# Kernel optimization log

Hardware: AMD Instinct MI355X
Metric: run time of the kernel (lower is better)

The kernel has to match this reference:

```python
import jax, jax.numpy as jnp
import numpy as np

N_NODES = 200000
N_EDGES = 6400000
IN_FEAT = 128
HIDDEN = 16


def gcn_conv(x, W, b, row, col, n):
    # PyG GCNConv: h = X W ; out_i = sum_{(j->i)} d_j^{-1/2} d_i^{-1/2} h_j + b
    # (row = source j, col = target i; self-loops already included in row/col)
    deg = jax.ops.segment_sum(jnp.ones_like(col, dtype=x.dtype), col, num_segments=n)
    dinv = jnp.where(deg > 0, jax.lax.rsqrt(deg), jnp.zeros_like(deg))
    norm = dinv[row] * dinv[col]            # [E+N]
    h = x @ W                               # [N, out] small GEMM
    msg = norm[:, None] * h[row]            # gather over edges
    out = jax.ops.segment_sum(msg, col, num_segments=n)  # scatter-add to targets
    return out + b


def setup_inputs() -> dict:
    key = jax.random.key(0)
    k1, k2, k3, k4 = jax.random.split(key, 4)
    x = jax.random.normal(k1, (N_NODES, IN_FEAT), dtype=jnp.float32)
    edge_index = jax.random.randint(k2, (2, N_EDGES), 0, N_NODES, dtype=jnp.int32)
    # Glorot-ish init for the two linear layers
    W1 = jax.random.normal(k3, (IN_FEAT, HIDDEN), dtype=jnp.float32) / np.sqrt(IN_FEAT)
    W2 = jax.random.normal(k4, (HIDDEN, 1), dtype=jnp.float32) / np.sqrt(HIDDEN)
    b1 = jnp.zeros((HIDDEN,), dtype=jnp.float32)
    b2 = jnp.zeros((1,), dtype=jnp.float32)
    return {"x": x, "edge_index": edge_index, "W1": W1, "b1": b1, "W2": W2, "b2": b2}


def reference(x, edge_index, W1, b1, W2, b2):
    n = x.shape[0]
    # add self-loops (as PyG GCNConv does by default)
    loop = jnp.arange(n, dtype=edge_index.dtype)
    row = jnp.concatenate([edge_index[0], loop])
    col = jnp.concatenate([edge_index[1], loop])
    h = gcn_conv(x, W1, b1, row, col, n)    # [N, 16]
    h = jax.nn.relu(h)
    out = gcn_conv(h, W2, b2, row, col, n)  # [N, 1]
    return out.squeeze(-1)                  # [N]
```

## Files before the change

kernel.cpp:

```cpp
#include <hip/hip_runtime.h>
#include <hip/hip_fp16.h>

#define N_NODES 200000
#define N_EDGES 6400000
#define IN_FEAT 128
#define HIDDEN  16

#define RN 128
#define NRF 1568
#define NC 98
#define CSHIFT 11
#define NPAD (NRF * RN)
#define SRC_MASK 0x3FFFFu
#define SB1 8192
#define SB2 8192
#define BPB 9
#define CAP 5120

typedef float v4f __attribute__((ext_vector_type(4)));
typedef _Float16 f16x8 __attribute__((ext_vector_type(8)));
typedef float f32x4 __attribute__((ext_vector_type(4)));


__global__ __launch_bounds__(512) void k_fcnt(const int* __restrict__ col,
                                              unsigned* __restrict__ fcnt) {
    __shared__ unsigned c[NRF];
    for (int i = threadIdx.x; i < NRF; i += 512) c[i] = 0u;
    __syncthreads();
    const int EPB = N_EDGES / 512;
    const int4* c4 = (const int4*)(col + (size_t)blockIdx.x * EPB);
    for (int i = threadIdx.x; i < EPB / 4; i += 512) {
        int4 v = c4[i];
        atomicAdd(&c[(unsigned)v.x >> 7], 1u);
        atomicAdd(&c[(unsigned)v.y >> 7], 1u);
        atomicAdd(&c[(unsigned)v.z >> 7], 1u);
        atomicAdd(&c[(unsigned)v.w >> 7], 1u);
    }
    __syncthreads();
    for (int i = threadIdx.x; i < NRF; i += 512)
        if (c[i]) atomicAdd(&fcnt[i], c[i]);
}


__global__ __launch_bounds__(1024) void k_scanr(const unsigned* __restrict__ fcnt,
                                                unsigned* __restrict__ foffs,
                                                unsigned* __restrict__ fcur,
                                                unsigned* __restrict__ coffs,
                                                unsigned* __restrict__ ccur) {
    __shared__ unsigned s[1024];
    const int t = threadIdx.x;
    unsigned c0 = (2 * t     < NRF) ? fcnt[2 * t]     : 0u;
    unsigned c1 = (2 * t + 1 < NRF) ? fcnt[2 * t + 1] : 0u;
    unsigned pairsum = c0 + c1;
    s[t] = pairsum;
    __syncthreads();
    #pragma unroll
    for (int d = 1; d < 1024; d <<= 1) {
        unsigned add = (t >= d) ? s[t - d] : 0u;
        __syncthreads();
        s[t] += add;
        __syncthreads();
    }
    unsigned excl = s[t] - pairsum;
    if (2 * t < NRF)     { foffs[2 * t]     = excl;      fcur[2 * t]     = excl; }
    if (2 * t + 1 < NRF) { foffs[2 * t + 1] = excl + c0; fcur[2 * t + 1] = excl + c0; }
    if (t == 1023) foffs[NRF] = s[t];
    __syncthreads();
    if (t < NC)  { unsigned v = foffs[16 * t]; coffs[t] = v; ccur[t] = v; }
    if (t == NC) coffs[NC] = N_EDGES;
}


__global__ __launch_bounds__(512) void k_cscat(const int* __restrict__ row,
                                               const int* __restrict__ col,
                                               unsigned* __restrict__ ccur,
                                               unsigned* __restrict__ tmp1) {
    __shared__ unsigned cnt[NC], gbase[NC], lcur[NC];
    const long long e0 = (long long)blockIdx.x * SB1;
    long long rem = (long long)N_EDGES - e0;
    const int n = rem > SB1 ? SB1 : (int)rem;
    if (threadIdx.x < NC) { cnt[threadIdx.x] = 0u; lcur[threadIdx.x] = 0u; }
    __syncthreads();
    const int4* c4 = (const int4*)(col + e0);
    const int4* r4 = (const int4*)(row + e0);
    for (int i = threadIdx.x; i < n / 4; i += 512) {
        int4 v = c4[i];
        atomicAdd(&cnt[(unsigned)v.x >> CSHIFT], 1u);
        atomicAdd(&cnt[(unsigned)v.y >> CSHIFT], 1u);
        atomicAdd(&cnt[(unsigned)v.z >> CSHIFT], 1u);
        atomicAdd(&cnt[(unsigned)v.w >> CSHIFT], 1u);
    }
    __syncthreads();
    if (threadIdx.x < NC)
        gbase[threadIdx.x] = cnt[threadIdx.x] ? atomicAdd(&ccur[threadIdx.x], cnt[threadIdx.x]) : 0u;
    __syncthreads();
    for (int i = threadIdx.x; i < n / 4; i += 512) {
        int4 c = c4[i];
        int4 r = r4[i];
        unsigned b, pos;
        b = (unsigned)c.x >> CSHIFT; pos = gbase[b] + atomicAdd(&lcur[b], 1u);
        tmp1[pos] = (((unsigned)c.x & 2047u) << 18) | (unsigned)r.x;
        b = (unsigned)c.y >> CSHIFT; pos = gbase[b] + atomicAdd(&lcur[b], 1u);
        tmp1[pos] = (((unsigned)c.y & 2047u) << 18) | (unsigned)r.y;
        b = (unsigned)c.z >> CSHIFT; pos = gbase[b] + atomicAdd(&lcur[b], 1u);
        tmp1[pos] = (((unsigned)c.z & 2047u) << 18) | (unsigned)r.z;
        b = (unsigned)c.w >> CSHIFT; pos = gbase[b] + atomicAdd(&lcur[b], 1u);
        tmp1[pos] = (((unsigned)c.w & 2047u) << 18) | (unsigned)r.w;
    }
}


__global__ __launch_bounds__(512) void k_fscat(const unsigned* __restrict__ tmp1,
                                               const unsigned* __restrict__ coffs,
                                               unsigned* __restrict__ fcur,
                                               unsigned* __restrict__ tmp2) {
    __shared__ unsigned cnt[16], gbase[16], lcur[16];
    const int b = blockIdx.x / BPB;
    const int sl = blockIdx.x % BPB;
    const unsigned blo = coffs[b], bhi = coffs[b + 1];
    const unsigned lo = blo + (unsigned)sl * SB2;
    if (lo >= bhi) return;
    const unsigned hi = (lo + SB2 < bhi) ? lo + SB2 : bhi;
    const unsigned n = hi - lo;
    if (threadIdx.x < 16) { cnt[threadIdx.x] = 0u; lcur[threadIdx.x] = 0u; }
    __syncthreads();
    for (unsigned i = threadIdx.x; i < n; i += 512)
        atomicAdd(&cnt[tmp1[lo + i] >> 25], 1u);
    __syncthreads();
    if (threadIdx.x < 16)
        gbase[threadIdx.x] = cnt[threadIdx.x]
            ? atomicAdd(&fcur[16 * b + threadIdx.x], cnt[threadIdx.x]) : 0u;
    __syncthreads();
    for (unsigned i = threadIdx.x; i < n; i += 512) {
        unsigned p = tmp1[lo + i];
        unsigned f = p >> 25;
        unsigned pos = gbase[f] + atomicAdd(&lcur[f], 1u);
        tmp2[pos] = p & 0x01FFFFFFu;
    }
}


__global__ __launch_bounds__(256) void k_bsort(const unsigned* __restrict__ tmp,
                                               const unsigned* __restrict__ boffs_r,
                                               unsigned* __restrict__ boffs_n,
                                               float* __restrict__ dinv,
                                               unsigned* __restrict__ sorted) {
    __shared__ unsigned obuf[CAP];
    __shared__ unsigned dcnt[RN], dcur[RN], sscan[RN];
    const int r = blockIdx.x;
    const unsigned lo = boffs_r[r], hi = boffs_r[r + 1];
    const unsigned cnt = hi - lo;
    const unsigned node0 = (unsigned)r * RN;
    if (threadIdx.x < RN) dcnt[threadIdx.x] = 0u;
    __syncthreads();

    for (unsigned i = threadIdx.x; i < cnt; i += 256)
        atomicAdd(&dcnt[tmp[lo + i] >> 18], 1u);
    __syncthreads();

    unsigned c = 0;
    if (threadIdx.x < RN) { c = dcnt[threadIdx.x]; sscan[threadIdx.x] = c; }
    __syncthreads();
    #pragma unroll
    for (int d = 1; d < RN; d <<= 1) {
        unsigned add = 0;
        if (threadIdx.x < RN && threadIdx.x >= d) add = sscan[threadIdx.x - d];
        __syncthreads();
        if (threadIdx.x < RN) sscan[threadIdx.x] += add;
        __syncthreads();
    }
    if (threadIdx.x < RN) {
        unsigned excl = sscan[threadIdx.x] - c;
        dcur[threadIdx.x] = excl;
        unsigned node = node0 + threadIdx.x;
        boffs_n[node] = lo + excl;
        if (node < N_NODES) dinv[node] = rsqrtf((float)c + 1.0f);
    }
    if (r == NRF - 1 && threadIdx.x == 0) boffs_n[NPAD] = hi;
    __syncthreads();

    if (cnt <= CAP) {
        for (unsigned i = threadIdx.x; i < cnt; i += 256) {
            unsigned p = tmp[lo + i];
            unsigned pos = atomicAdd(&dcur[p >> 18], 1u);
            obuf[pos] = p & SRC_MASK;
        }
        __syncthreads();
        for (unsigned i = threadIdx.x; i < cnt; i += 256)
            sorted[lo + i] = obuf[i];
    } else {
        for (unsigned i = threadIdx.x; i < cnt; i += 256) {
            unsigned p = tmp[lo + i];
            unsigned pos = atomicAdd(&dcur[p >> 18], 1u);
            sorted[lo + pos] = p & SRC_MASK;
        }
    }
}


__global__ __launch_bounds__(256) void k_gemm1(const float* __restrict__ x,
                                               const float* __restrict__ W1,
                                               const float* __restrict__ dinv,
                                               __half* __restrict__ h16) {
    const int wave = (blockIdx.x * 256 + threadIdx.x) >> 6;
    const int lane = threadIdx.x & 63;
    const int m16 = lane & 15;
    const int quad = lane >> 4;
    if (wave * 16 >= N_NODES) return;

    f16x8 bf[4];
    #pragma unroll
    for (int kb = 0; kb < 4; ++kb)
        #pragma unroll
        for (int j = 0; j < 8; ++j)
            bf[kb][j] = (_Float16)W1[(kb * 32 + quad * 8 + j) * HIDDEN + m16];

    const int node0 = wave * 16;
    const float* xrow = x + (size_t)(node0 + m16) * IN_FEAT + quad * 8;
    f32x4 acc = {0.f, 0.f, 0.f, 0.f};
    #pragma unroll
    for (int kb = 0; kb < 4; ++kb) {
        const v4f* p = (const v4f*)(xrow + kb * 32);
        v4f u0 = p[0], u1 = p[1];
        f16x8 af;
        af[0] = (_Float16)u0.x; af[1] = (_Float16)u0.y;
        af[2] = (_Float16)u0.z; af[3] = (_Float16)u0.w;
        af[4] = (_Float16)u1.x; af[5] = (_Float16)u1.y;
        af[6] = (_Float16)u1.z; af[7] = (_Float16)u1.w;
        acc = __builtin_amdgcn_mfma_f32_16x16x32_f16(af, bf[kb], acc, 0, 0, 0);
    }
    #pragma unroll
    for (int r = 0; r < 4; ++r) {
        int node = node0 + quad * 4 + r;
        h16[(size_t)node * HIDDEN + m16] = __float2half(dinv[node] * acc[r]);
    }
}


__global__ __launch_bounds__(256) void k_agg1(const unsigned* __restrict__ sorted,
                                              const unsigned* __restrict__ boffs,
                                              const unsigned* __restrict__ h16u,
                                              const float* __restrict__ dinv,
                                              const float* __restrict__ b1,
                                              const float* __restrict__ W2,
                                              float* __restrict__ tp) {
    const unsigned tid = blockIdx.x * 256 + threadIdx.x;
    const unsigned node = tid >> 3;
    const int l = tid & 7;
    if (node >= N_NODES) return;

    unsigned e = boffs[node];
    const unsigned o1 = boffs[node + 1];
    float ax = 0.f, ay = 0.f;

    unsigned n0, n1, n2, n3, n4, n5, n6, n7;
    bool have = (e + 8 <= o1);
    if (have) {
        n0 = sorted[e];     n1 = sorted[e + 1]; n2 = sorted[e + 2]; n3 = sorted[e + 3];
        n4 = sorted[e + 4]; n5 = sorted[e + 5]; n6 = sorted[e + 6]; n7 = sorted[e + 7];
    }
    while (have) {
        unsigned c0 = n0, c1 = n1, c2 = n2, c3 = n3, c4 = n4, c5 = n5, c6 = n6, c7 = n7;
        e += 8;
        have = (e + 8 <= o1);
        if (have) {
            n0 = sorted[e];     n1 = sorted[e + 1]; n2 = sorted[e + 2]; n3 = sorted[e + 3];
            n4 = sorted[e + 4]; n5 = sorted[e + 5]; n6 = sorted[e + 6]; n7 = sorted[e + 7];
        }
        unsigned v0 = h16u[(size_t)c0 * 8 + l];
        unsigned v1 = h16u[(size_t)c1 * 8 + l];
        unsigned v2 = h16u[(size_t)c2 * 8 + l];
        unsigned v3 = h16u[(size_t)c3 * 8 + l];
        unsigned v4 = h16u[(size_t)c4 * 8 + l];
        unsigned v5 = h16u[(size_t)c5 * 8 + l];
        unsigned v6 = h16u[(size_t)c6 * 8 + l];
        unsigned v7 = h16u[(size_t)c7 * 8 + l];
        float2 f0 = __half22float2(*(const __half2*)&v0);
        float2 f1 = __half22float2(*(const __half2*)&v1);
        float2 f2 = __half22float2(*(const __half2*)&v2);
        float2 f3 = __half22float2(*(const __half2*)&v3);
        float2 f4 = __half22float2(*(const __half2*)&v4);
        float2 f5 = __half22float2(*(const __half2*)&v5);
        float2 f6 = __half22float2(*(const __half2*)&v6);
        float2 f7 = __half22float2(*(const __half2*)&v7);
        ax += f0.x + f1.x + f2.x + f3.x;
        ay += f0.y + f1.y + f2.y + f3.y;
        ax += f4.x + f5.x + f6.x + f7.x;
        ay += f4.y + f5.y + f6.y + f7.y;
    }
    for (; e < o1; ++e) {
        unsigned s = sorted[e];
        unsigned v = h16u[(size_t)s * 8 + l];
        float2 f = __half22float2(*(const __half2*)&v);
        ax += f.x; ay += f.y;
    }

    unsigned vs = h16u[(size_t)node * 8 + l];
    float2 fs = __half22float2(*(const __half2*)&vs);
    float di = dinv[node];
    float px = fmaf(di, ax + fs.x, b1[2 * l]);
    float py = fmaf(di, ay + fs.y, b1[2 * l + 1]);
    float r = fmaxf(px, 0.f) * W2[2 * l] + fmaxf(py, 0.f) * W2[2 * l + 1];
    r += __shfl_xor(r, 4, 8);
    r += __shfl_xor(r, 2, 8);
    r += __shfl_xor(r, 1, 8);
    if (l == 0) tp[node] = di * r;
}


__global__ __launch_bounds__(256) void k_agg2(const unsigned* __restrict__ sorted,
                                              const unsigned* __restrict__ boffs,
                                              const float* __restrict__ tp,
                                              const float* __restrict__ dinv,
                                              const float* __restrict__ b2,
                                              float* __restrict__ out) {
    const unsigned node = blockIdx.x * 256 + threadIdx.x;
    if (node >= N_NODES) return;

    unsigned e = boffs[node];
    const unsigned o1 = boffs[node + 1];
    float acc = 0.f;

    unsigned n0, n1, n2, n3, n4, n5, n6, n7;
    bool have = (e + 8 <= o1);
    if (have) {
        n0 = sorted[e];     n1 = sorted[e + 1]; n2 = sorted[e + 2]; n3 = sorted[e + 3];
        n4 = sorted[e + 4]; n5 = sorted[e + 5]; n6 = sorted[e + 6]; n7 = sorted[e + 7];
    }
    while (have) {
        unsigned c0 = n0, c1 = n1, c2 = n2, c3 = n3, c4 = n4, c5 = n5, c6 = n6, c7 = n7;
        e += 8;
        have = (e + 8 <= o1);
        if (have) {
            n0 = sorted[e];     n1 = sorted[e + 1]; n2 = sorted[e + 2]; n3 = sorted[e + 3];
            n4 = sorted[e + 4]; n5 = sorted[e + 5]; n6 = sorted[e + 6]; n7 = sorted[e + 7];
        }
        float t0 = tp[c0], t1 = tp[c1], t2 = tp[c2], t3 = tp[c3];
        float t4 = tp[c4], t5 = tp[c5], t6 = tp[c6], t7 = tp[c7];
        acc += t0 + t1 + t2 + t3;
        acc += t4 + t5 + t6 + t7;
    }
    for (; e < o1; ++e) acc += tp[sorted[e]];

    out[node] = fmaf(dinv[node], tp[node] + acc, b2[0]);
}


extern "C" void kernel_launch(void* const* d_in, const int* in_sizes, int n_in,
                              void* d_out, int out_size, void* d_ws, size_t ws_size,
                              hipStream_t stream) {
    const float* x   = (const float*)d_in[0];
    const int*   ei  = (const int*)d_in[1];
    const float* W1  = (const float*)d_in[2];
    const float* b1  = (const float*)d_in[3];
    const float* W2  = (const float*)d_in[4];
    const float* b2  = (const float*)d_in[5];
    float* out = (float*)d_out;

    const int* row = ei;
    const int* col = ei + N_EDGES;

    unsigned* fcnt    = (unsigned*)d_ws;
    unsigned* foffs   = fcnt + 2048;
    unsigned* fcur    = foffs + 2048;
    unsigned* coffs   = fcur + 2048;
    unsigned* ccur    = coffs + 128;
    unsigned* boffs_n = ccur + 128;
    float*    dinv    = (float*)(boffs_n + NPAD + 64);
    float*    tp      = dinv + N_NODES;
    __half*   h16     = (__half*)(tp + N_NODES);
    unsigned* tmp1    = (unsigned*)(h16 + (size_t)N_NODES * HIDDEN);
    unsigned* tmp2    = tmp1 + N_EDGES;
    unsigned* sorted  = tmp1;

    (void)hipMemsetAsync(fcnt, 0, 2048 * sizeof(unsigned), stream);
    k_fcnt<<<512, 512, 0, stream>>>(col, fcnt);
    k_scanr<<<1, 1024, 0, stream>>>(fcnt, foffs, fcur, coffs, ccur);
    k_cscat<<<(N_EDGES + SB1 - 1) / SB1, 512, 0, stream>>>(row, col, ccur, tmp1);
    k_fscat<<<NC * BPB, 512, 0, stream>>>(tmp1, coffs, fcur, tmp2);
    k_bsort<<<NRF, 256, 0, stream>>>(tmp2, foffs, boffs_n, dinv, sorted);
    k_gemm1<<<(N_NODES / 16 + 3) / 4, 256, 0, stream>>>(x, W1, dinv, h16);
    k_agg1<<<(N_NODES * 8) / 256 + 1, 256, 0, stream>>>(sorted, boffs_n, (const unsigned*)h16,
                                                        dinv, b1, W2, tp);
    k_agg2<<<(N_NODES + 255) / 256, 256, 0, stream>>>(sorted, boffs_n, tp, dinv, b2, out);
}
```

Before: 409.8 us.

## Collapse three-level radix sort into two passes with 512-node buckets

Replaces the coarse-scatter / fine-scatter / per-128-node sort pipeline with a two-pass scheme: edges are scattered into 391 buckets of 512 target nodes, then one 1024-thread block per bucket counts per node and scatters sources directly to global memory. This removes one full read and write pass over the edge array and a kernel launch. The scatter kernel also keeps the loaded col/row vectors in registers between counting and writing instead of re-reading them. The cost is fewer, larger sort blocks (391) with uncoalesced global writes instead of LDS staging, plus more buckets contending on atomics in the coarse scatter.

```diff
diff --git a/kernel.cpp b/kernel.cpp
--- a/kernel.cpp
+++ b/kernel.cpp
@@ -6,68 +6,54 @@
 #define IN_FEAT 128
 #define HIDDEN  16
 
-#define RN 128
-#define NRF 1568
-#define NC 98
-#define CSHIFT 11
-#define NPAD (NRF * RN)
+#define RN 512
+#define CSHIFT 9
+#define NC 391
+#define NPAD (NC * RN)
 #define SRC_MASK 0x3FFFFu
-#define SB1 8192
-#define SB2 8192
-#define BPB 9
-#define CAP 5120
+#define SB1 4096
 
 typedef float v4f __attribute__((ext_vector_type(4)));
 typedef _Float16 f16x8 __attribute__((ext_vector_type(8)));
 typedef float f32x4 __attribute__((ext_vector_type(4)));
 
 
-__global__ __launch_bounds__(512) void k_fcnt(const int* __restrict__ col,
-                                              unsigned* __restrict__ fcnt) {
-    __shared__ unsigned c[NRF];
-    for (int i = threadIdx.x; i < NRF; i += 512) c[i] = 0u;
+__global__ __launch_bounds__(512) void k_ccnt(const int* __restrict__ col,
+                                              unsigned* __restrict__ ccnt) {
+    __shared__ unsigned c[NC];
+    if (threadIdx.x < NC) c[threadIdx.x] = 0u;
     __syncthreads();
     const int EPB = N_EDGES / 512;
     const int4* c4 = (const int4*)(col + (size_t)blockIdx.x * EPB);
     for (int i = threadIdx.x; i < EPB / 4; i += 512) {
         int4 v = c4[i];
-        atomicAdd(&c[(unsigned)v.x >> 7], 1u);
-        atomicAdd(&c[(unsigned)v.y >> 7], 1u);
-        atomicAdd(&c[(unsigned)v.z >> 7], 1u);
-        atomicAdd(&c[(unsigned)v.w >> 7], 1u);
-    }
-    __syncthreads();
-    for (int i = threadIdx.x; i < NRF; i += 512)
-        if (c[i]) atomicAdd(&fcnt[i], c[i]);
-}
-
-
-__global__ __launch_bounds__(1024) void k_scanr(const unsigned* __restrict__ fcnt,
-                                                unsigned* __restrict__ foffs,
-                                                unsigned* __restrict__ fcur,
-                                                unsigned* __restrict__ coffs,
-                                                unsigned* __restrict__ ccur) {
-    __shared__ unsigned s[1024];
+        atomicAdd(&c[(unsigned)v.x >> CSHIFT], 1u);
+        atomicAdd(&c[(unsigned)v.y >> CSHIFT], 1u);
+        atomicAdd(&c[(unsigned)v.z >> CSHIFT], 1u);
+        atomicAdd(&c[(unsigned)v.w >> CSHIFT], 1u);
+    }
+    __syncthreads();
+    if (threadIdx.x < NC && c[threadIdx.x]) atomicAdd(&ccnt[threadIdx.x], c[threadIdx.x]);
+}
+
+
+__global__ __launch_bounds__(512) void k_scanc(const unsigned* __restrict__ ccnt,
+                                               unsigned* __restrict__ coffs,
+                                               unsigned* __restrict__ ccur) {
+    __shared__ unsigned s[512];
     const int t = threadIdx.x;
-    unsigned c0 = (2 * t     < NRF) ? fcnt[2 * t]     : 0u;
-    unsigned c1 = (2 * t + 1 < NRF) ? fcnt[2 * t + 1] : 0u;
-    unsigned pairsum = c0 + c1;
-    s[t] = pairsum;
-    __syncthreads();
-    #pragma unroll
-    for (int d = 1; d < 1024; d <<= 1) {
+    unsigned v = (t < NC) ? ccnt[t] : 0u;
+    s[t] = v;
+    __syncthreads();
+    #pragma unroll
+    for (int d = 1; d < 512; d <<= 1) {
         unsigned add = (t >= d) ? s[t - d] : 0u;
         __syncthreads();
         s[t] += add;
         __syncthreads();
     }
-    unsigned excl = s[t] - pairsum;
-    if (2 * t < NRF)     { foffs[2 * t]     = excl;      fcur[2 * t]     = excl; }
-    if (2 * t + 1 < NRF) { foffs[2 * t + 1] = excl + c0; fcur[2 * t + 1] = excl + c0; }
-    if (t == 1023) foffs[NRF] = s[t];
-    __syncthreads();
-    if (t < NC)  { unsigned v = foffs[16 * t]; coffs[t] = v; ccur[t] = v; }
-    if (t == NC) coffs[NC] = N_EDGES;
+    if (t < NC) { unsigned e = s[t] - v; coffs[t] = e; ccur[t] = e; }
+    if (t == NC - 1) coffs[NC] = s[t];
 }
 
 
@@ -83,8 +69,13 @@
     __syncthreads();
     const int4* c4 = (const int4*)(col + e0);
     const int4* r4 = (const int4*)(row + e0);
-    for (int i = threadIdx.x; i < n / 4; i += 512) {
+    const int n4 = n / 4;
+    int4 cc[2], rr[2];
+    int nit = 0;
+    for (int i = threadIdx.x; i < n4; i += 512, ++nit) {
         int4 v = c4[i];
+        cc[nit] = v;
+        rr[nit] = r4[i];
         atomicAdd(&cnt[(unsigned)v.x >> CSHIFT], 1u);
         atomicAdd(&cnt[(unsigned)v.y >> CSHIFT], 1u);
         atomicAdd(&cnt[(unsigned)v.z >> CSHIFT], 1u);
@@ -94,68 +85,36 @@
     if (threadIdx.x < NC)
         gbase[threadIdx.x] = cnt[threadIdx.x] ? atomicAdd(&ccur[threadIdx.x], cnt[threadIdx.x]) : 0u;
     __syncthreads();
-    for (int i = threadIdx.x; i < n / 4; i += 512) {
-        int4 c = c4[i];
-        int4 r = r4[i];
+    for (int it = 0; it < nit; ++it) {
+        int4 c = cc[it];
+        int4 r = rr[it];
         unsigned b, pos;
         b = (unsigned)c.x >> CSHIFT; pos = gbase[b] + atomicAdd(&lcur[b], 1u);
-        tmp1[pos] = (((unsigned)c.x & 2047u) << 18) | (unsigned)r.x;
+        tmp1[pos] = (((unsigned)c.x & (RN - 1u)) << 18) | (unsigned)r.x;
         b = (unsigned)c.y >> CSHIFT; pos = gbase[b] + atomicAdd(&lcur[b], 1u);
-        tmp1[pos] = (((unsigned)c.y & 2047u) << 18) | (unsigned)r.y;
+        tmp1[pos] = (((unsigned)c.y & (RN - 1u)) << 18) | (unsigned)r.y;
         b = (unsigned)c.z >> CSHIFT; pos = gbase[b] + atomicAdd(&lcur[b], 1u);
-        tmp1[pos] = (((unsigned)c.z & 2047u) << 18) | (unsigned)r.z;
+        tmp1[pos] = (((unsigned)c.z & (RN - 1u)) << 18) | (unsigned)r.z;
         b = (unsigned)c.w >> CSHIFT; pos = gbase[b] + atomicAdd(&lcur[b], 1u);
-        tmp1[pos] = (((unsigned)c.w & 2047u) << 18) | (unsigned)r.w;
-    }
-}
-
-
-__global__ __launch_bounds__(512) void k_fscat(const unsigned* __restrict__ tmp1,
-                                               const unsigned* __restrict__ coffs,
-                                               unsigned* __restrict__ fcur,
-                                               unsigned* __restrict__ tmp2) {
-    __shared__ unsigned cnt[16], gbase[16], lcur[16];
-    const int b = blockIdx.x / BPB;
-    const int sl = blockIdx.x % BPB;
-    const unsigned blo = coffs[b], bhi = coffs[b + 1];
-    const unsigned lo = blo + (unsigned)sl * SB2;
-    if (lo >= bhi) return;
-    const unsigned hi = (lo + SB2 < bhi) ? lo + SB2 : bhi;
-    const unsigned n = hi - lo;
-    if (threadIdx.x < 16) { cnt[threadIdx.x] = 0u; lcur[threadIdx.x] = 0u; }
-    __syncthreads();
-    for (unsigned i = threadIdx.x; i < n; i += 512)
-        atomicAdd(&cnt[tmp1[lo + i] >> 25], 1u);
-    __syncthreads();
-    if (threadIdx.x < 16)
-        gbase[threadIdx.x] = cnt[threadIdx.x]
-            ? atomicAdd(&fcur[16 * b + threadIdx.x], cnt[threadIdx.x]) : 0u;
-    __syncthreads();
-    for (unsigned i = threadIdx.x; i < n; i += 512) {
-        unsigned p = tmp1[lo + i];
-        unsigned f = p >> 25;
-        unsigned pos = gbase[f] + atomicAdd(&lcur[f], 1u);
-        tmp2[pos] = p & 0x01FFFFFFu;
-    }
-}
-
-
-__global__ __launch_bounds__(256) void k_bsort(const unsigned* __restrict__ tmp,
-                                               const unsigned* __restrict__ boffs_r,
-                                               unsigned* __restrict__ boffs_n,
-                                               float* __restrict__ dinv,
-                                               unsigned* __restrict__ sorted) {
-    __shared__ unsigned obuf[CAP];
+        tmp1[pos] = (((unsigned)c.w & (RN - 1u)) << 18) | (unsigned)r.w;
+    }
+}
+
+
+__global__ __launch_bounds__(1024) void k_bsort(const unsigned* __restrict__ tmp1,
+                                                const unsigned* __restrict__ coffs,
+                                                unsigned* __restrict__ boffs_n,
+                                                float* __restrict__ dinv,
+                                                unsigned* __restrict__ sorted) {
     __shared__ unsigned dcnt[RN], dcur[RN], sscan[RN];
     const int r = blockIdx.x;
-    const unsigned lo = boffs_r[r], hi = boffs_r[r + 1];
-    const unsigned cnt = hi - lo;
+    const unsigned lo = coffs[r], hi = coffs[r + 1];
     const unsigned node0 = (unsigned)r * RN;
     if (threadIdx.x < RN) dcnt[threadIdx.x] = 0u;
     __syncthreads();
 
-    for (unsigned i = threadIdx.x; i < cnt; i += 256)
-        atomicAdd(&dcnt[tmp[lo + i] >> 18], 1u);
+    for (unsigned i = lo + threadIdx.x; i < hi; i += 1024)
+        atomicAdd(&dcnt[tmp1[i] >> 18], 1u);
     __syncthreads();
 
     unsigned c = 0;
@@ -176,24 +135,28 @@
         boffs_n[node] = lo + excl;
         if (node < N_NODES) dinv[node] = rsqrtf((float)c + 1.0f);
     }
-    if (r == NRF - 1 && threadIdx.x == 0) boffs_n[NPAD] = hi;
-    __syncthreads();
-
-    if (cnt <= CAP) {
-        for (unsigned i = threadIdx.x; i < cnt; i += 256) {
-            unsigned p = tmp[lo + i];
-            unsigned pos = atomicAdd(&dcur[p >> 18], 1u);
-            obuf[pos] = p & SRC_MASK;
-        }
-        __syncthreads();
-        for (unsigned i = threadIdx.x; i < cnt; i += 256)
-            sorted[lo + i] = obuf[i];
-    } else {
-        for (unsigned i = threadIdx.x; i < cnt; i += 256) {
-            unsigned p = tmp[lo + i];
-            unsigned pos = atomicAdd(&dcur[p >> 18], 1u);
-            sorted[lo + pos] = p & SRC_MASK;
-        }
+    if (r == NC - 1 && threadIdx.x == 0) boffs_n[NPAD] = hi;
+    __syncthreads();
+
+    unsigned i = lo + threadIdx.x;
+    for (; i + 3072 < hi; i += 4096) {
+        unsigned p0 = tmp1[i];
+        unsigned p1 = tmp1[i + 1024];
+        unsigned p2 = tmp1[i + 2048];
+        unsigned p3 = tmp1[i + 3072];
+        unsigned q0 = atomicAdd(&dcur[p0 >> 18], 1u);
+        unsigned q1 = atomicAdd(&dcur[p1 >> 18], 1u);
+        unsigned q2 = atomicAdd(&dcur[p2 >> 18], 1u);
+        unsigned q3 = atomicAdd(&dcur[p3 >> 18], 1u);
+        sorted[lo + q0] = p0 & SRC_MASK;
+        sorted[lo + q1] = p1 & SRC_MASK;
+        sorted[lo + q2] = p2 & SRC_MASK;
+        sorted[lo + q3] = p3 & SRC_MASK;
+    }
+    for (; i < hi; i += 1024) {
+        unsigned p = tmp1[i];
+        unsigned pos = atomicAdd(&dcur[p >> 18], 1u);
+        sorted[lo + pos] = p & SRC_MASK;
     }
 }
 
@@ -360,25 +323,21 @@
     const int* row = ei;
     const int* col = ei + N_EDGES;
 
-    unsigned* fcnt    = (unsigned*)d_ws;
-    unsigned* foffs   = fcnt + 2048;
-    unsigned* fcur    = foffs + 2048;
-    unsigned* coffs   = fcur + 2048;
-    unsigned* ccur    = coffs + 128;
-    unsigned* boffs_n = ccur + 128;
+    unsigned* ccnt    = (unsigned*)d_ws;
+    unsigned* coffs   = ccnt + 512;
+    unsigned* ccur    = coffs + 512;
+    unsigned* boffs_n = ccur + 512;
     float*    dinv    = (float*)(boffs_n + NPAD + 64);
     float*    tp      = dinv + N_NODES;
     __half*   h16     = (__half*)(tp + N_NODES);
     unsigned* tmp1    = (unsigned*)(h16 + (size_t)N_NODES * HIDDEN);
-    unsigned* tmp2    = tmp1 + N_EDGES;
-    unsigned* sorted  = tmp1;
-
-    (void)hipMemsetAsync(fcnt, 0, 2048 * sizeof(unsigned), stream);
-    k_fcnt<<<512, 512, 0, stream>>>(col, fcnt);
-    k_scanr<<<1, 1024, 0, stream>>>(fcnt, foffs, fcur, coffs, ccur);
+    unsigned* sorted  = tmp1 + N_EDGES;
+
+    (void)hipMemsetAsync(ccnt, 0, 512 * sizeof(unsigned), stream);
+    k_ccnt<<<512, 512, 0, stream>>>(col, ccnt);
+    k_scanc<<<1, 512, 0, stream>>>(ccnt, coffs, ccur);
     k_cscat<<<(N_EDGES + SB1 - 1) / SB1, 512, 0, stream>>>(row, col, ccur, tmp1);
-    k_fscat<<<NC * BPB, 512, 0, stream>>>(tmp1, coffs, fcur, tmp2);
-    k_bsort<<<NRF, 256, 0, stream>>>(tmp2, foffs, boffs_n, dinv, sorted);
+    k_bsort<<<NC, 1024, 0, stream>>>(tmp1, coffs, boffs_n, dinv, sorted);
     k_gemm1<<<(N_NODES / 16 + 3) / 4, 256, 0, stream>>>(x, W1, dinv, h16);
     k_agg1<<<(N_NODES * 8) / 256 + 1, 256, 0, stream>>>(sorted, boffs_n, (const unsigned*)h16,
                                                         dinv, b1, W2, tp);
```

Result: no change. 414.8 us (+1.2%).
